# Optimization experiments

Measured on AMD Instinct MI355X. Metric: run time of the kernel, lower is better.

## Reference

```python
import jax, jax.numpy as jnp
import numpy as np

N_RES = 384
PAIR_DIM = 128
NUM_HEAD = 4
KEY_DIM = PAIR_DIM // NUM_HEAD  # 32
LN_EPS = 1e-5


def setup_inputs() -> dict:
    key = jax.random.key(0)
    ks = jax.random.split(key, 12)
    s = 0.02
    return {
        "pair_act": jax.random.normal(ks[0], (N_RES, N_RES, PAIR_DIM), jnp.float32),
        "pair_mask": jnp.ones((N_RES, N_RES), jnp.float32),
        "ln_scale": jnp.ones((PAIR_DIM,), jnp.float32),
        "ln_bias": jnp.zeros((PAIR_DIM,), jnp.float32),
        "feat2d_w": jax.random.normal(ks[1], (PAIR_DIM, NUM_HEAD), jnp.float32) * s,
        "q_w": jax.random.normal(ks[2], (PAIR_DIM, NUM_HEAD, KEY_DIM), jnp.float32) * s,
        "k_w": jax.random.normal(ks[3], (PAIR_DIM, NUM_HEAD, KEY_DIM), jnp.float32) * s,
        "v_w": jax.random.normal(ks[4], (PAIR_DIM, NUM_HEAD, KEY_DIM), jnp.float32) * s,
        "gate_w": jax.random.normal(ks[5], (PAIR_DIM, NUM_HEAD, KEY_DIM), jnp.float32) * s,
        "gate_b": jnp.ones((NUM_HEAD, KEY_DIM), jnp.float32),  # AF2 gating bias init = 1
        "o_w": jax.random.normal(ks[6], (NUM_HEAD, KEY_DIM, PAIR_DIM), jnp.float32) * s,
        "o_b": jnp.zeros((PAIR_DIM,), jnp.float32),
    }


def reference(pair_act, pair_mask, ln_scale, ln_bias, feat2d_w,
              q_w, k_w, v_w, gate_w, gate_b, o_w, o_b):
    # orientation == 'per_row': no transpose.
    # mask bias: [B, 1, 1, K] with B = rows, K = keys (columns)
    bias = (1e9 * (pair_mask - 1.0))[:, None, None, :]

    # LayerNorm over channel dim
    mu = jnp.mean(pair_act, axis=-1, keepdims=True)
    var = jnp.mean(jnp.square(pair_act - mu), axis=-1, keepdims=True)
    x = (pair_act - mu) * jax.lax.rsqrt(var + LN_EPS) * ln_scale + ln_bias

    # nonbatched triangle bias: [q, k, c] @ [c, h] -> permute to [h, q, k]
    nb_bias = jnp.einsum('qkc,ch->hqk', x, feat2d_w)

    # AF2 attention (q_data = m_data = x), per-row batched
    q = jnp.einsum('bqa,ahc->bqhc', x, q_w) * (KEY_DIM ** -0.5)
    k = jnp.einsum('bka,ahc->bkhc', x, k_w)
    v = jnp.einsum('bka,ahc->bkhc', x, v_w)

    logits = jnp.einsum('bqhc,bkhc->bhqk', q, k) + bias + nb_bias[None]
    weights = jax.nn.softmax(logits, axis=-1)
    weighted = jnp.einsum('bhqk,bkhc->bqhc', weights, v)

    gate = jax.nn.sigmoid(jnp.einsum('bqa,ahc->bqhc', x, gate_w) + gate_b)
    weighted = weighted * gate

    out = jnp.einsum('bqhc,hco->bqo', weighted, o_w) + o_b
    return out
```

## Files before the change

### kernel.cpp

```cpp
#include <hip/hip_runtime.h>

typedef __attribute__((ext_vector_type(8))) short v8s;
typedef __attribute__((ext_vector_type(4))) float v4f;
typedef unsigned short u16;
typedef unsigned int u32;

#define NRES 384
#define NN (NRES*NRES)
#define QKVE (NN*128)

__device__ __forceinline__ u16 f2b(float f){
  u32 u = __builtin_bit_cast(u32, f);
  u += 0x7FFFu + ((u>>16)&1u);
  return (u16)(u>>16);
}
__device__ __forceinline__ float b2f(u16 h){
  u32 u = ((u32)h)<<16;
  return __builtin_bit_cast(float, u);
}
__device__ __forceinline__ int swz256(int row, int colb){
  return (row*256 + colb) ^ ((row&7)<<4);
}
__device__ __forceinline__ int swz768(int row, int colb){
  return (row*768 + colb) ^ ((row&7)<<4);
}

__global__ __launch_bounds__(256) void k_prep_w(
    const float* __restrict__ qw, const float* __restrict__ kw,
    const float* __restrict__ vw, const float* __restrict__ gw,
    const float* __restrict__ ow, u16* __restrict__ wts){
  int gid = blockIdx.x*256 + threadIdx.x;
  int m = gid >> 14, r = gid & 16383;
  int n = r >> 7, a = r & 127;
  const float* src = (m==0)?qw:((m==1)?kw:((m==2)?vw:((m==3)?gw:ow)));
  float v = src[a*128 + n];
  if (m==0) v *= 0.17677669529663687f;
  wts[gid] = f2b(v);
}

__global__ __launch_bounds__(256) void k_ln_proj(
    const float* __restrict__ X, const float* __restrict__ lns,
    const float* __restrict__ lnb, const float* __restrict__ f2w,
    const float* __restrict__ gb, const u16* __restrict__ wts,
    u16* __restrict__ qbuf, u16* __restrict__ kbuf,
    u16* __restrict__ vT, u16* __restrict__ gbuf, u16* __restrict__ nbb){
  __shared__ __align__(16) u16 Xs[128*128];
  int tid = threadIdx.x;
  int blk = blockIdx.x;
  int p0 = blk*128;
  int bi = blk/3;
  int j0 = (blk%3)*128;

  {
    int row = tid>>1;
    int half = (tid&1)*64;
    const float4* xp4 = (const float4*)(X + (size_t)(p0+row)*128 + half);
    float4 v[16];
    float s=0.f, ss=0.f;
    #pragma unroll
    for (int i=0;i<16;i++){ v[i]=xp4[i];
      s  += v[i].x+v[i].y+v[i].z+v[i].w;
      ss += v[i].x*v[i].x+v[i].y*v[i].y+v[i].z*v[i].z+v[i].w*v[i].w; }
    s += __shfl_xor(s,1); ss += __shfl_xor(ss,1);
    float mu = s*(1.f/128.f);
    float rstd = rsqrtf(ss*(1.f/128.f) - mu*mu + 1e-5f);
    float nb0=0,nb1=0,nb2=0,nb3=0;
    #pragma unroll
    for (int i=0;i<16;i++){
      int c = half + i*4;
      float4 sc = *(const float4*)(lns+c);
      float4 bi4= *(const float4*)(lnb+c);
      float xn0 = (v[i].x-mu)*rstd*sc.x + bi4.x;
      float xn1 = (v[i].y-mu)*rstd*sc.y + bi4.y;
      float xn2 = (v[i].z-mu)*rstd*sc.z + bi4.z;
      float xn3 = (v[i].w-mu)*rstd*sc.w + bi4.w;
      float4 fw0 = *(const float4*)(f2w + (c+0)*4);
      float4 fw1 = *(const float4*)(f2w + (c+1)*4);
      float4 fw2 = *(const float4*)(f2w + (c+2)*4);
      float4 fw3 = *(const float4*)(f2w + (c+3)*4);
      nb0 += xn0*fw0.x + xn1*fw1.x + xn2*fw2.x + xn3*fw3.x;
      nb1 += xn0*fw0.y + xn1*fw1.y + xn2*fw2.y + xn3*fw3.y;
      nb2 += xn0*fw0.z + xn1*fw1.z + xn2*fw2.z + xn3*fw3.z;
      nb3 += xn0*fw0.w + xn1*fw1.w + xn2*fw2.w + xn3*fw3.w;
      u32 pk0 = (u32)f2b(xn0) | ((u32)f2b(xn1)<<16);
      u32 pk1 = (u32)f2b(xn2) | ((u32)f2b(xn3)<<16);
      *(u32*)((char*)Xs + swz256(row, c*2))   = pk0;
      *(u32*)((char*)Xs + swz256(row, c*2+4)) = pk1;
    }
    nb0 += __shfl_xor(nb0,1); nb1 += __shfl_xor(nb1,1);
    nb2 += __shfl_xor(nb2,1); nb3 += __shfl_xor(nb3,1);
    if ((tid&1)==0){
      int pos = bi*NRES + j0 + row;
      nbb[0*NN+pos]=f2b(nb0); nbb[1*NN+pos]=f2b(nb1);
      nbb[2*NN+pos]=f2b(nb2); nbb[3*NN+pos]=f2b(nb3);
    }
  }
  __syncthreads();

  int wv = tid>>6, lane = tid&63, l15 = lane&15, lhi = lane>>4;
  const v4f z4 = {0.f,0.f,0.f,0.f};
  for (int mi=0; mi<4; mi++){
    int m = mi; if (mi==2) m=3; else if (mi==3) m=2;
    v4f acc[8][2];
    #pragma unroll
    for (int mf=0;mf<8;mf++){ acc[mf][0]=z4; acc[mf][1]=z4; }
    for (int ks=0; ks<4; ks++){
      v8s af[8];
      #pragma unroll
      for (int mf=0;mf<8;mf++)
        af[mf] = *(const v8s*)((char*)Xs + swz256(mf*16+l15, (ks*32+lhi*8)*2));
      v8s bf[2];
      #pragma unroll
      for (int nf=0;nf<2;nf++)
        bf[nf] = *(const v8s*)(wts + m*16384 + (wv*32+nf*16+l15)*128 + ks*32 + lhi*8);
      #pragma unroll
      for (int mf=0;mf<8;mf++){
        acc[mf][0] = __builtin_amdgcn_mfma_f32_16x16x32_bf16(af[mf], bf[0], acc[mf][0],0,0,0);
        acc[mf][1] = __builtin_amdgcn_mfma_f32_16x16x32_bf16(af[mf], bf[1], acc[mf][1],0,0,0);
      }
    }
    if (mi==3){
      __syncthreads();
      #pragma unroll
      for (int mf=0;mf<8;mf++)
        #pragma unroll
        for (int nf=0;nf<2;nf++)
          #pragma unroll
          for (int r=0;r<4;r++){
            int pr = mf*16 + lhi*4 + r;
            int n  = wv*32 + nf*16 + l15;
            *(u16*)((char*)Xs + swz256(n, pr*2)) = f2b(acc[mf][nf][r]);
          }
      __syncthreads();
      int n = tid>>1, jh = (tid&1)*64;
      int hh = n>>5, d = n&31;
      u16* dst = vT + (size_t)((bi*4+hh)*32 + d)*NRES + j0 + jh;
      #pragma unroll
      for (int i=0;i<32;i++){
        u32 val = *(u32*)((char*)Xs + swz256(n, (jh+i*2)*2));
        *(u32*)(dst + i*2) = val;
      }
    } else {
      u16* outp = (m==0)?qbuf:((m==1)?kbuf:gbuf);
      #pragma unroll
      for (int mf=0;mf<8;mf++)
        #pragma unroll
        for (int nf=0;nf<2;nf++){
          int n = wv*32 + nf*16 + l15;
          #pragma unroll
          for (int r=0;r<4;r++){
            int pr = mf*16 + lhi*4 + r;
            float val = acc[mf][nf][r];
            if (m==3) val = 1.f/(1.f+__expf(-(val + gb[n])));
            outp[(size_t)(p0+pr)*128 + n] = f2b(val);
          }
        }
    }
  }
}

__global__ __launch_bounds__(256) void k_attn(
    u16* qwg,
    const u16* __restrict__ kbuf, const u16* __restrict__ vT,
    const u16* __restrict__ gbuf, const u16* __restrict__ nbb,
    const float* __restrict__ mask){
  __shared__ __align__(16) char smem[49152];
  __shared__ float red[4][64];
  __shared__ float rowmax[64];
  __shared__ float rowsum[64];
  int tid = threadIdx.x;
  int qt = blockIdx.x, h = blockIdx.y, b = blockIdx.z;
  int q0 = qt*64;
  int wv = tid>>6, lane = tid&63, l15 = lane&15, lhi = lane>>4;
  const v4f z4 = {0.f,0.f,0.f,0.f};

  v8s qa[4];
  #pragma unroll
  for (int mf=0;mf<4;mf++)
    qa[mf] = *(const v8s*)(qwg + (size_t)(b*NRES + q0 + mf*16 + l15)*128 + h*32 + lhi*8);
  v4f s[4][6];
  #pragma unroll
  for (int mf=0;mf<4;mf++)
    #pragma unroll
    for (int nf=0;nf<6;nf++) s[mf][nf]=z4;
  #pragma unroll
  for (int nf=0;nf<6;nf++){
    int key = wv*96 + nf*16 + l15;
    v8s kb = *(const v8s*)(kbuf + (size_t)(b*NRES + key)*128 + h*32 + lhi*8);
    #pragma unroll
    for (int mf=0;mf<4;mf++)
      s[mf][nf] = __builtin_amdgcn_mfma_f32_16x16x32_bf16(qa[mf], kb, s[mf][nf],0,0,0);
  }
  #pragma unroll
  for (int nf=0;nf<6;nf++){
    int key = wv*96 + nf*16 + l15;
    float mb = 1e9f*(mask[b*NRES+key]-1.f);
    #pragma unroll
    for (int mf=0;mf<4;mf++)
      #pragma unroll
      for (int r=0;r<4;r++){
        int qr = q0 + mf*16 + lhi*4 + r;
        s[mf][nf][r] += mb + b2f(nbb[h*NN + qr*NRES + key]);
      }
  }
  #pragma unroll
  for (int mf=0;mf<4;mf++)
    #pragma unroll
    for (int r=0;r<4;r++){
      float m = s[mf][0][r];
      #pragma unroll
      for (int nf=1;nf<6;nf++) m = fmaxf(m, s[mf][nf][r]);
      m = fmaxf(m, __shfl_xor(m,1)); m = fmaxf(m, __shfl_xor(m,2));
      m = fmaxf(m, __shfl_xor(m,4)); m = fmaxf(m, __shfl_xor(m,8));
      if (l15==0) red[wv][mf*16+lhi*4+r] = m;
    }
  __syncthreads();
  if (tid<64) rowmax[tid] = fmaxf(fmaxf(red[0][tid],red[1][tid]),fmaxf(red[2][tid],red[3][tid]));
  __syncthreads();
  #pragma unroll
  for (int mf=0;mf<4;mf++)
    #pragma unroll
    for (int r=0;r<4;r++){
      int rowl = mf*16+lhi*4+r;
      float mx = rowmax[rowl];
      float sum = 0.f;
      #pragma unroll
      for (int nf=0;nf<6;nf++){
        float p = __expf(s[mf][nf][r] - mx);
        sum += p;
        int key = wv*96 + nf*16 + l15;
        *(u16*)(smem + swz768(rowl, key*2)) = f2b(p);
      }
      sum += __shfl_xor(sum,1); sum += __shfl_xor(sum,2);
      sum += __shfl_xor(sum,4); sum += __shfl_xor(sum,8);
      if (l15==0) red[wv][rowl] = sum;
    }
  __syncthreads();
  if (tid<64) rowsum[tid] = red[0][tid]+red[1][tid]+red[2][tid]+red[3][tid];
  __syncthreads();
  v4f o[4][2];
  #pragma unroll
  for (int mf=0;mf<4;mf++){ o[mf][0]=z4; o[mf][1]=z4; }
  #pragma unroll
  for (int ks=0;ks<3;ks++){
    int key0 = wv*96 + ks*32;
    v8s pa[4];
    #pragma unroll
    for (int mf=0;mf<4;mf++)
      pa[mf] = *(const v8s*)(smem + swz768(mf*16+l15, (key0+lhi*8)*2));
    v8s vb[2];
    #pragma unroll
    for (int nf=0;nf<2;nf++)
      vb[nf] = *(const v8s*)(vT + (size_t)((b*4+h)*32 + nf*16 + l15)*NRES + key0 + lhi*8);
    #pragma unroll
    for (int mf=0;mf<4;mf++){
      o[mf][0] = __builtin_amdgcn_mfma_f32_16x16x32_bf16(pa[mf], vb[0], o[mf][0],0,0,0);
      o[mf][1] = __builtin_amdgcn_mfma_f32_16x16x32_bf16(pa[mf], vb[1], o[mf][1],0,0,0);
    }
  }
  __syncthreads();
  float* outred = (float*)smem;
  #pragma unroll
  for (int mf=0;mf<4;mf++)
    #pragma unroll
    for (int nf=0;nf<2;nf++)
      #pragma unroll
      for (int r=0;r<4;r++)
        outred[wv*2112 + (mf*16+lhi*4+r)*33 + nf*16+l15] = o[mf][nf][r];
  __syncthreads();
  int rowl = tid>>2, d0 = (tid&3)*8;
  float inv = 1.f/rowsum[rowl];
  size_t base = (size_t)(b*NRES + q0 + rowl)*128 + h*32;
  #pragma unroll
  for (int i=0;i<8;i++){
    int d = d0+i;
    float sv = outred[0*2112+rowl*33+d] + outred[1*2112+rowl*33+d]
             + outred[2*2112+rowl*33+d] + outred[3*2112+rowl*33+d];
    float g = b2f(gbuf[base + d]);
    qwg[base + d] = f2b(sv*inv*g);
  }
}

__global__ __launch_bounds__(256) void k_outproj(
    const u16* __restrict__ wg, const u16* __restrict__ wts,
    const float* __restrict__ ob, float* __restrict__ out){
  int tid = threadIdx.x;
  int p0 = blockIdx.x*128;
  int wv = tid>>6, lane = tid&63, l15 = lane&15, lhi = lane>>4;
  const v4f z4 = {0.f,0.f,0.f,0.f};
  v4f acc[8][2];
  #pragma unroll
  for (int mf=0;mf<8;mf++){ acc[mf][0]=z4; acc[mf][1]=z4; }
  const u16* wo = wts + 4*16384;
  #pragma unroll
  for (int ks=0;ks<4;ks++){
    v8s af[8];
    #pragma unroll
    for (int mf=0;mf<8;mf++)
      af[mf] = *(const v8s*)(wg + (size_t)(p0+mf*16+l15)*128 + ks*32 + lhi*8);
    v8s bf[2];
    #pragma unroll
    for (int nf=0;nf<2;nf++)
      bf[nf] = *(const v8s*)(wo + (wv*32+nf*16+l15)*128 + ks*32 + lhi*8);
    #pragma unroll
    for (int mf=0;mf<8;mf++){
      acc[mf][0] = __builtin_amdgcn_mfma_f32_16x16x32_bf16(af[mf], bf[0], acc[mf][0],0,0,0);
      acc[mf][1] = __builtin_amdgcn_mfma_f32_16x16x32_bf16(af[mf], bf[1], acc[mf][1],0,0,0);
    }
  }
  #pragma unroll
  for (int nf=0;nf<2;nf++){
    int n = wv*32 + nf*16 + l15;
    float obn = ob[n];
    #pragma unroll
    for (int mf=0;mf<8;mf++)
      #pragma unroll
      for (int r=0;r<4;r++)
        out[(size_t)(p0+mf*16+lhi*4+r)*128 + n] = acc[mf][nf][r] + obn;
  }
}

extern "C" void kernel_launch(void* const* d_in, const int* in_sizes, int n_in,
                              void* d_out, int out_size, void* d_ws, size_t ws_size,
                              hipStream_t stream){
  const float* pair_act = (const float*)d_in[0];
  const float* pair_mask= (const float*)d_in[1];
  const float* ln_scale = (const float*)d_in[2];
  const float* ln_bias  = (const float*)d_in[3];
  const float* f2w      = (const float*)d_in[4];
  const float* q_w      = (const float*)d_in[5];
  const float* k_w      = (const float*)d_in[6];
  const float* v_w      = (const float*)d_in[7];
  const float* g_w      = (const float*)d_in[8];
  const float* g_b      = (const float*)d_in[9];
  const float* o_w      = (const float*)d_in[10];
  const float* o_b      = (const float*)d_in[11];
  float* out = (float*)d_out;

  u16* qbuf = (u16*)d_ws;
  u16* kbuf = qbuf + (size_t)QKVE;
  u16* vT   = kbuf + (size_t)QKVE;
  u16* gbuf = vT   + (size_t)QKVE;
  u16* nbb  = gbuf + (size_t)QKVE;
  u16* wts  = nbb  + (size_t)(4*NN);

  hipLaunchKernelGGL(k_prep_w, dim3(320), dim3(256), 0, stream,
                     q_w, k_w, v_w, g_w, o_w, wts);
  hipLaunchKernelGGL(k_ln_proj, dim3(1152), dim3(256), 0, stream,
                     pair_act, ln_scale, ln_bias, f2w, g_b, wts,
                     qbuf, kbuf, vT, gbuf, nbb);
  hipLaunchKernelGGL(k_attn, dim3(6,4,384), dim3(256), 0, stream,
                     qbuf, kbuf, vT, gbuf, nbb, pair_mask);
  hipLaunchKernelGGL(k_outproj, dim3(1152), dim3(256), 0, stream,
                     qbuf, wts, o_b, out);
}
```

Baseline: 758.2 us.

## Restructure attention so each wave owns 16 queries across all heads

The attention kernel is rewritten so each wave computes the full 384-key softmax for 16 queries in registers, computing S^T (keys x queries) with MFMA and feeding probabilities straight into a 16x16x16 MFMA against V. This removes the shared-memory P staging, the cross-wave max/sum reductions and the output reduction with their barriers. The nonbatched bias is stored in a new interleaved layout so each lane reads four contiguous values, and that bias plus the mask preloaded into LDS is fed in as the MFMA accumulator init. Blocks are remapped so neighbouring (row, query-tile) work lands on the same XCD, and heads are looped inside each block. The cost is higher register pressure from 24 live accumulators, a launch-bounds occupancy hint, and less parallelism per block.

```diff
diff --git a/kernel.cpp b/kernel.cpp
--- a/kernel.cpp
+++ b/kernel.cpp
@@ -1,6 +1,7 @@
 #include <hip/hip_runtime.h>
 
 typedef __attribute__((ext_vector_type(8))) short v8s;
+typedef __attribute__((ext_vector_type(4))) short v4s;
 typedef __attribute__((ext_vector_type(4))) float v4f;
 typedef unsigned short u16;
 typedef unsigned int u32;
@@ -21,8 +22,14 @@
 __device__ __forceinline__ int swz256(int row, int colb){
   return (row*256 + colb) ^ ((row&7)<<4);
 }
-__device__ __forceinline__ int swz768(int row, int colb){
-  return (row*768 + colb) ^ ((row&7)<<4);
+__device__ __forceinline__ v4f mfma16(v4s a, v4s b, v4f c){
+#if __has_builtin(__builtin_amdgcn_mfma_f32_16x16x16bf16_1k)
+  return __builtin_amdgcn_mfma_f32_16x16x16bf16_1k(a, b, c, 0, 0, 0);
+#else
+  v4f d;
+  asm("v_mfma_f32_16x16x16_bf16 %0, %1, %2, %3" : "=v"(d) : "v"(a), "v"(b), "v"(c));
+  return d;
+#endif
 }
 
 __global__ __launch_bounds__(256) void k_prep_w(
@@ -90,9 +97,10 @@
     nb0 += __shfl_xor(nb0,1); nb1 += __shfl_xor(nb1,1);
     nb2 += __shfl_xor(nb2,1); nb3 += __shfl_xor(nb3,1);
     if ((tid&1)==0){
-      int pos = bi*NRES + j0 + row;
-      nbb[0*NN+pos]=f2b(nb0); nbb[1*NN+pos]=f2b(nb1);
-      nbb[2*NN+pos]=f2b(nb2); nbb[3*NN+pos]=f2b(nb3);
+      int k = j0 + row;
+      int base2 = ((k>>2)*NRES + bi)*4 + (k&3);
+      nbb[0*NN+base2]=f2b(nb0); nbb[1*NN+base2]=f2b(nb1);
+      nbb[2*NN+base2]=f2b(nb2); nbb[3*NN+base2]=f2b(nb3);
     }
   }
   __syncthreads();
@@ -159,125 +167,84 @@
   }
 }
 
-__global__ __launch_bounds__(256) void k_attn(
+__global__ __launch_bounds__(256,3) void k_attn(
     u16* qwg,
     const u16* __restrict__ kbuf, const u16* __restrict__ vT,
     const u16* __restrict__ gbuf, const u16* __restrict__ nbb,
     const float* __restrict__ mask){
-  __shared__ __align__(16) char smem[49152];
-  __shared__ float red[4][64];
-  __shared__ float rowmax[64];
-  __shared__ float rowsum[64];
+  __shared__ float lmask[NRES];
   int tid = threadIdx.x;
-  int qt = blockIdx.x, h = blockIdx.y, b = blockIdx.z;
+  int bid = blockIdx.x;
+  int xcd = bid & 7, li = bid >> 3;
+  int t = xcd*288 + li;
+  int b = t/6, qt = t - b*6;
   int q0 = qt*64;
+  for (int i = tid; i < NRES; i += 256)
+    lmask[i] = 1e9f*(mask[b*NRES + i] - 1.0f);
+  __syncthreads();
+
   int wv = tid>>6, lane = tid&63, l15 = lane&15, lhi = lane>>4;
+  int q0t = q0 + wv*16;
   const v4f z4 = {0.f,0.f,0.f,0.f};
 
-  v8s qa[4];
-  #pragma unroll
-  for (int mf=0;mf<4;mf++)
-    qa[mf] = *(const v8s*)(qwg + (size_t)(b*NRES + q0 + mf*16 + l15)*128 + h*32 + lhi*8);
-  v4f s[4][6];
-  #pragma unroll
-  for (int mf=0;mf<4;mf++)
-    #pragma unroll
-    for (int nf=0;nf<6;nf++) s[mf][nf]=z4;
-  #pragma unroll
-  for (int nf=0;nf<6;nf++){
-    int key = wv*96 + nf*16 + l15;
-    v8s kb = *(const v8s*)(kbuf + (size_t)(b*NRES + key)*128 + h*32 + lhi*8);
-    #pragma unroll
-    for (int mf=0;mf<4;mf++)
-      s[mf][nf] = __builtin_amdgcn_mfma_f32_16x16x32_bf16(qa[mf], kb, s[mf][nf],0,0,0);
-  }
-  #pragma unroll
-  for (int nf=0;nf<6;nf++){
-    int key = wv*96 + nf*16 + l15;
-    float mb = 1e9f*(mask[b*NRES+key]-1.f);
-    #pragma unroll
-    for (int mf=0;mf<4;mf++)
-      #pragma unroll
-      for (int r=0;r<4;r++){
-        int qr = q0 + mf*16 + lhi*4 + r;
-        s[mf][nf][r] += mb + b2f(nbb[h*NN + qr*NRES + key]);
+  for (int h=0; h<4; h++){
+    v8s qb = *(const v8s*)(qwg + (size_t)(b*NRES + q0t + l15)*128 + h*32 + lhi*8);
+    v4f s[24];
+    #pragma unroll
+    for (int mf=0; mf<24; mf++){
+      v4s nb4 = *(const v4s*)(nbb + (size_t)h*NN + ((mf*4+lhi)*NRES + q0t + l15)*4);
+      float4 mb4 = *(const float4*)&lmask[mf*16 + lhi*4];
+      v4f c;
+      c[0] = mb4.x + b2f((u16)nb4[0]);
+      c[1] = mb4.y + b2f((u16)nb4[1]);
+      c[2] = mb4.z + b2f((u16)nb4[2]);
+      c[3] = mb4.w + b2f((u16)nb4[3]);
+      v8s ka = *(const v8s*)(kbuf + (size_t)(b*NRES + mf*16 + l15)*128 + h*32 + lhi*8);
+      s[mf] = __builtin_amdgcn_mfma_f32_16x16x32_bf16(ka, qb, c, 0,0,0);
+    }
+    float m0=-1e30f, m1=-1e30f, m2=-1e30f, m3=-1e30f;
+    #pragma unroll
+    for (int mf=0; mf<24; mf++){
+      m0 = fmaxf(m0, s[mf][0]); m1 = fmaxf(m1, s[mf][1]);
+      m2 = fmaxf(m2, s[mf][2]); m3 = fmaxf(m3, s[mf][3]);
+    }
+    float mx = fmaxf(fmaxf(m0,m1), fmaxf(m2,m3));
+    mx = fmaxf(mx, __shfl_xor(mx,16));
+    mx = fmaxf(mx, __shfl_xor(mx,32));
+    v4f oe0=z4, oe1=z4, oo0=z4, oo1=z4;
+    float se=0.f, so=0.f;
+    const u16* vbase = vT + (size_t)((b*4+h)*32)*NRES;
+    #pragma unroll
+    for (int mf=0; mf<24; mf++){
+      float p0 = __expf(s[mf][0]-mx), p1 = __expf(s[mf][1]-mx);
+      float p2 = __expf(s[mf][2]-mx), p3 = __expf(s[mf][3]-mx);
+      v4s pa;
+      pa[0]=(short)f2b(p0); pa[1]=(short)f2b(p1);
+      pa[2]=(short)f2b(p2); pa[3]=(short)f2b(p3);
+      v4s vb0 = *(const v4s*)(vbase + (size_t)(l15)*NRES      + mf*16 + lhi*4);
+      v4s vb1 = *(const v4s*)(vbase + (size_t)(16+l15)*NRES   + mf*16 + lhi*4);
+      if (mf & 1){
+        so += (p0+p1)+(p2+p3);
+        oo0 = mfma16(pa, vb0, oo0);
+        oo1 = mfma16(pa, vb1, oo1);
+      } else {
+        se += (p0+p1)+(p2+p3);
+        oe0 = mfma16(pa, vb0, oe0);
+        oe1 = mfma16(pa, vb1, oe1);
       }
-  }
-  #pragma unroll
-  for (int mf=0;mf<4;mf++)
-    #pragma unroll
-    for (int r=0;r<4;r++){
-      float m = s[mf][0][r];
-      #pragma unroll
-      for (int nf=1;nf<6;nf++) m = fmaxf(m, s[mf][nf][r]);
-      m = fmaxf(m, __shfl_xor(m,1)); m = fmaxf(m, __shfl_xor(m,2));
-      m = fmaxf(m, __shfl_xor(m,4)); m = fmaxf(m, __shfl_xor(m,8));
-      if (l15==0) red[wv][mf*16+lhi*4+r] = m;
-    }
-  __syncthreads();
-  if (tid<64) rowmax[tid] = fmaxf(fmaxf(red[0][tid],red[1][tid]),fmaxf(red[2][tid],red[3][tid]));
-  __syncthreads();
-  #pragma unroll
-  for (int mf=0;mf<4;mf++)
-    #pragma unroll
-    for (int r=0;r<4;r++){
-      int rowl = mf*16+lhi*4+r;
-      float mx = rowmax[rowl];
-      float sum = 0.f;
-      #pragma unroll
-      for (int nf=0;nf<6;nf++){
-        float p = __expf(s[mf][nf][r] - mx);
-        sum += p;
-        int key = wv*96 + nf*16 + l15;
-        *(u16*)(smem + swz768(rowl, key*2)) = f2b(p);
-      }
-      sum += __shfl_xor(sum,1); sum += __shfl_xor(sum,2);
-      sum += __shfl_xor(sum,4); sum += __shfl_xor(sum,8);
-      if (l15==0) red[wv][rowl] = sum;
-    }
-  __syncthreads();
-  if (tid<64) rowsum[tid] = red[0][tid]+red[1][tid]+red[2][tid]+red[3][tid];
-  __syncthreads();
-  v4f o[4][2];
-  #pragma unroll
-  for (int mf=0;mf<4;mf++){ o[mf][0]=z4; o[mf][1]=z4; }
-  #pragma unroll
-  for (int ks=0;ks<3;ks++){
-    int key0 = wv*96 + ks*32;
-    v8s pa[4];
-    #pragma unroll
-    for (int mf=0;mf<4;mf++)
-      pa[mf] = *(const v8s*)(smem + swz768(mf*16+l15, (key0+lhi*8)*2));
-    v8s vb[2];
-    #pragma unroll
-    for (int nf=0;nf<2;nf++)
-      vb[nf] = *(const v8s*)(vT + (size_t)((b*4+h)*32 + nf*16 + l15)*NRES + key0 + lhi*8);
-    #pragma unroll
-    for (int mf=0;mf<4;mf++){
-      o[mf][0] = __builtin_amdgcn_mfma_f32_16x16x32_bf16(pa[mf], vb[0], o[mf][0],0,0,0);
-      o[mf][1] = __builtin_amdgcn_mfma_f32_16x16x32_bf16(pa[mf], vb[1], o[mf][1],0,0,0);
-    }
-  }
-  __syncthreads();
-  float* outred = (float*)smem;
-  #pragma unroll
-  for (int mf=0;mf<4;mf++)
-    #pragma unroll
-    for (int nf=0;nf<2;nf++)
-      #pragma unroll
-      for (int r=0;r<4;r++)
-        outred[wv*2112 + (mf*16+lhi*4+r)*33 + nf*16+l15] = o[mf][nf][r];
-  __syncthreads();
-  int rowl = tid>>2, d0 = (tid&3)*8;
-  float inv = 1.f/rowsum[rowl];
-  size_t base = (size_t)(b*NRES + q0 + rowl)*128 + h*32;
-  #pragma unroll
-  for (int i=0;i<8;i++){
-    int d = d0+i;
-    float sv = outred[0*2112+rowl*33+d] + outred[1*2112+rowl*33+d]
-             + outred[2*2112+rowl*33+d] + outred[3*2112+rowl*33+d];
-    float g = b2f(gbuf[base + d]);
-    qwg[base + d] = f2b(sv*inv*g);
+    }
+    float sum = se + so;
+    sum += __shfl_xor(sum,16); sum += __shfl_xor(sum,32);
+    v4f o0 = oe0 + oo0, o1 = oe1 + oo1;
+    #pragma unroll
+    for (int r=0; r<4; r++){
+      float rinv = 1.f/__shfl(sum, lhi*4+r);
+      size_t base = (size_t)(b*NRES + q0t + lhi*4 + r)*128 + h*32;
+      float g0 = b2f(gbuf[base + l15]);
+      float g1 = b2f(gbuf[base + 16 + l15]);
+      qwg[base + l15]      = f2b(o0[r]*rinv*g0);
+      qwg[base + 16 + l15] = f2b(o1[r]*rinv*g1);
+    }
   }
 }
 
@@ -349,7 +316,7 @@
   hipLaunchKernelGGL(k_ln_proj, dim3(1152), dim3(256), 0, stream,
                      pair_act, ln_scale, ln_bias, f2w, g_b, wts,
                      qbuf, kbuf, vT, gbuf, nbb);
-  hipLaunchKernelGGL(k_attn, dim3(6,4,384), dim3(256), 0, stream,
+  hipLaunchKernelGGL(k_attn, dim3(2304), dim3(256), 0, stream,
                      qbuf, kbuf, vT, gbuf, nbb, pair_mask);
   hipLaunchKernelGGL(k_outproj, dim3(1152), dim3(256), 0, stream,
                      qbuf, wts, o_b, out);
```

After: 965.0 us. 1.27x slower.
